# Kernel optimization log

Hardware: AMD Instinct MI355X
Metric: run time of the kernel (lower is better)

## Reference

```python
import jax, jax.numpy as jnp
import numpy as np
from jax import lax


def _bayer_kernels():
    # 5 fixed 3x3 interpolation stencils (identity, plus-avg, cross-avg, h-avg, v-avg)
    k5 = np.array([
        [[0, 0, 0], [0, 1, 0], [0, 0, 0]],
        [[0, .25, 0], [.25, 0, .25], [0, .25, 0]],
        [[.25, 0, .25], [0, 0, 0], [.25, 0, .25]],
        [[0, 0, 0], [.5, 0, .5], [0, 0, 0]],
        [[0, .5, 0], [0, 0, 0], [0, .5, 0]],
    ], dtype=np.float32)  # (5,3,3)
    # 4 fixed (3,5) selection matrices (1x1 convs per Bayer quadrant)
    sel = np.array([
        [[0, 0, 1, 0, 0], [0, 1, 0, 0, 0], [1, 0, 0, 0, 0]],
        [[0, 0, 0, 0, 1], [1, 0, 0, 0, 0], [0, 0, 0, 1, 0]],
        [[0, 0, 0, 1, 0], [1, 0, 0, 0, 0], [0, 0, 0, 0, 1]],
        [[1, 0, 0, 0, 0], [0, 1, 0, 0, 0], [0, 0, 1, 0, 0]],
    ], dtype=np.float32)  # (4,3,5)
    return jnp.asarray(k5), jnp.asarray(sel)


def setup_inputs() -> dict:
    key = jax.random.key(0)
    x = jax.random.uniform(key, (2, 1, 4096, 4096), dtype=jnp.float32) * 255.0
    k5, sel = _bayer_kernels()
    return {"x": x, "kernels5": k5, "sel": sel}


def reference(x, kernels5, sel):
    n, _, h, w = x.shape
    x_pad = jnp.pad(x, ((0, 0), (0, 0), (1, 1), (1, 1)), mode="reflect")
    # 3x3 stencil bank: (N,1,H+2,W+2) -> (N,5,H,W)
    xc = lax.conv_general_dilated(
        x_pad, kernels5.reshape(5, 1, 3, 3), window_strides=(1, 1),
        padding="VALID", dimension_numbers=("NCHW", "OIHW", "NCHW"))
    h2, w2 = h // 2, w // 2
    # pixel-unshuffle (DCR order): (N,5,H,W) -> (N, 2,2, 5, H/2, W/2) -> (N,4,5,H/2,W/2)
    u = xc.reshape(n, 5, h2, 2, w2, 2).transpose(0, 3, 5, 1, 2, 4).reshape(n, 4, 5, h2, w2)
    # per-quadrant 1x1 selection conv: (N,4,3,H/2,W/2)
    e = jnp.einsum("qos,nqsxy->nqoxy", sel, u)
    # pixel-shuffle (DCR order): (N,4,3,H/2,W/2) -> (N,3,H,W)
    y = e.reshape(n, 2, 2, 3, h2, w2).transpose(0, 3, 4, 1, 5, 2).reshape(n, 3, h, w)
    return y
```

## Files before the change

kernel.cpp:

```cpp
#include <hip/hip_runtime.h>


#define IMG_H 4096
#define IMG_W 4096

typedef float v4f __attribute__((ext_vector_type(4)));

__device__ __forceinline__ void load_win(const float* __restrict__ rowp, int j,
                                         int lane, float w[6]) {
    const float4 v = *(const float4*)(rowp + j);
    w[1] = v.x; w[2] = v.y; w[3] = v.z; w[4] = v.w;
    float left  = __shfl_up(v.w, 1);
    float right = __shfl_down(v.x, 1);
    if (lane == 0)  left  = (j == 0) ? v.y : rowp[j - 1];
    if (lane == 63) right = (j == IMG_W - 4) ? v.z : rowp[j + 4];
    w[0] = left; w[5] = right;
}

__global__ __launch_bounds__(256) void bayer_demosaic_kernel(
    const float* __restrict__ x, float* __restrict__ out) {
    const int jg   = blockIdx.x * blockDim.x + threadIdx.x;
    const int r    = blockIdx.y << 1;
    const int n    = blockIdx.z;
    const int j    = jg << 2;
    const int lane = threadIdx.x & 63;

    const float* xn = x + (size_t)n * IMG_H * IMG_W;

    const int rm = (r == 0) ? 1 : r - 1;
    const int rp = (r == IMG_H - 2) ? IMG_H - 2 : r + 2;

    const float* rowA = xn + (size_t)rm * IMG_W;
    const float* rowB = xn + (size_t)r  * IMG_W;
    const float* rowC = xn + (size_t)(r + 1) * IMG_W;
    const float* rowD = xn + (size_t)rp * IMG_W;

    float a[6], b[6], c[6], d[6];
    load_win(rowA, j, lane, a);
    load_win(rowB, j, lane, b);
    load_win(rowC, j, lane, c);
    load_win(rowD, j, lane, d);

    float e0[4], e1[4], e2[4];
    float f0[4], f1[4], f2[4];
#pragma unroll
    for (int k = 0; k < 4; ++k) {
        {
            const float center = b[k + 1];
            const float plus   = 0.25f * (a[k + 1] + c[k + 1] + b[k] + b[k + 2]);
            const float cross  = 0.25f * (a[k] + a[k + 2] + c[k] + c[k + 2]);
            const float havg   = 0.5f  * (b[k] + b[k + 2]);
            const float vavg   = 0.5f  * (a[k + 1] + c[k + 1]);
            if ((k & 1) == 0) { e0[k] = cross; e1[k] = plus;   e2[k] = center; }
            else              { e0[k] = vavg;  e1[k] = center; e2[k] = havg;   }
        }
        {
            const float center = c[k + 1];
            const float plus   = 0.25f * (b[k + 1] + d[k + 1] + c[k] + c[k + 2]);
            const float cross  = 0.25f * (b[k] + b[k + 2] + d[k] + d[k + 2]);
            const float havg   = 0.5f  * (c[k] + c[k + 2]);
            const float vavg   = 0.5f  * (b[k + 1] + d[k + 1]);
            if ((k & 1) == 0) { f0[k] = havg;   f1[k] = center; f2[k] = vavg;  }
            else              { f0[k] = center; f1[k] = plus;   f2[k] = cross; }
        }
    }

    float* on = out + (size_t)n * 3 * IMG_H * IMG_W;
    const size_t plane = (size_t)IMG_H * IMG_W;
    const size_t off0  = (size_t)r * IMG_W + j;
    const size_t off1  = off0 + IMG_W;

    v4f t;
    t = (v4f){e0[0], e0[1], e0[2], e0[3]};
    __builtin_nontemporal_store(t, (v4f*)(on + off0));
    t = (v4f){f0[0], f0[1], f0[2], f0[3]};
    __builtin_nontemporal_store(t, (v4f*)(on + off1));
    t = (v4f){e1[0], e1[1], e1[2], e1[3]};
    __builtin_nontemporal_store(t, (v4f*)(on + plane + off0));
    t = (v4f){f1[0], f1[1], f1[2], f1[3]};
    __builtin_nontemporal_store(t, (v4f*)(on + plane + off1));
    t = (v4f){e2[0], e2[1], e2[2], e2[3]};
    __builtin_nontemporal_store(t, (v4f*)(on + 2 * plane + off0));
    t = (v4f){f2[0], f2[1], f2[2], f2[3]};
    __builtin_nontemporal_store(t, (v4f*)(on + 2 * plane + off1));
}

extern "C" void kernel_launch(void* const* d_in, const int* in_sizes, int n_in,
                              void* d_out, int out_size, void* d_ws, size_t ws_size,
                              hipStream_t stream) {
    const float* x = (const float*)d_in[0];
    float* out = (float*)d_out;

    const int N = 2;
    dim3 block(256, 1, 1);
    dim3 grid(IMG_W / 4 / 256, IMG_H / 2, N);
    bayer_demosaic_kernel<<<grid, block, 0, stream>>>(x, out);
}
```

Measured before the change: 488.6 us.

## Process multiple row pairs per thread with sliding window reuse

Each thread now loops over several consecutive row pairs and carries the previous two rows' windows forward, so each input row is loaded about once instead of twice. The grid's y-dimension shrinks accordingly. Output stores switch from nontemporal builtins to plain float4 stores. This reduces redundant global/L2 reads and per-block overhead, but lowers parallelism and may change write caching behaviour.

```diff
diff --git a/kernel.cpp b/kernel.cpp
--- a/kernel.cpp
+++ b/kernel.cpp
@@ -3,8 +3,7 @@
 
 #define IMG_H 4096
 #define IMG_W 4096
-
-typedef float v4f __attribute__((ext_vector_type(4)));
+#define T_PAIRS 8
 
 __device__ __forceinline__ void load_win(const float* __restrict__ rowp, int j,
                                          int lane, float w[6]) {
@@ -20,69 +19,64 @@
 __global__ __launch_bounds__(256) void bayer_demosaic_kernel(
     const float* __restrict__ x, float* __restrict__ out) {
     const int jg   = blockIdx.x * blockDim.x + threadIdx.x;
-    const int r    = blockIdx.y << 1;
-    const int n    = blockIdx.z;
     const int j    = jg << 2;
     const int lane = threadIdx.x & 63;
+    const int n    = blockIdx.z;
+    int r = blockIdx.y * (2 * T_PAIRS);
 
     const float* xn = x + (size_t)n * IMG_H * IMG_W;
+    float* on       = out + (size_t)n * 3 * IMG_H * IMG_W;
+    const size_t plane = (size_t)IMG_H * IMG_W;
 
-    const int rm = (r == 0) ? 1 : r - 1;
-    const int rp = (r == IMG_H - 2) ? IMG_H - 2 : r + 2;
-
-    const float* rowA = xn + (size_t)rm * IMG_W;
-    const float* rowB = xn + (size_t)r  * IMG_W;
-    const float* rowC = xn + (size_t)(r + 1) * IMG_W;
-    const float* rowD = xn + (size_t)rp * IMG_W;
-
-    float a[6], b[6], c[6], d[6];
-    load_win(rowA, j, lane, a);
-    load_win(rowB, j, lane, b);
-    load_win(rowC, j, lane, c);
-    load_win(rowD, j, lane, d);
-
-    float e0[4], e1[4], e2[4];
-    float f0[4], f1[4], f2[4];
-#pragma unroll
-    for (int k = 0; k < 4; ++k) {
-        {
-            const float center = b[k + 1];
-            const float plus   = 0.25f * (a[k + 1] + c[k + 1] + b[k] + b[k + 2]);
-            const float cross  = 0.25f * (a[k] + a[k + 2] + c[k] + c[k + 2]);
-            const float havg   = 0.5f  * (b[k] + b[k + 2]);
-            const float vavg   = 0.5f  * (a[k + 1] + c[k + 1]);
-            if ((k & 1) == 0) { e0[k] = cross; e1[k] = plus;   e2[k] = center; }
-            else              { e0[k] = vavg;  e1[k] = center; e2[k] = havg;   }
-        }
-        {
-            const float center = c[k + 1];
-            const float plus   = 0.25f * (b[k + 1] + d[k + 1] + c[k] + c[k + 2]);
-            const float cross  = 0.25f * (b[k] + b[k + 2] + d[k] + d[k + 2]);
-            const float havg   = 0.5f  * (c[k] + c[k + 2]);
-            const float vavg   = 0.5f  * (b[k + 1] + d[k + 1]);
-            if ((k & 1) == 0) { f0[k] = havg;   f1[k] = center; f2[k] = vavg;  }
-            else              { f0[k] = center; f1[k] = plus;   f2[k] = cross; }
-        }
+    float A[6], B[6], C[6], D[6];
+    {
+        const int rm = (r == 0) ? 1 : r - 1;
+        load_win(xn + (size_t)rm * IMG_W, j, lane, A);
+        load_win(xn + (size_t)r  * IMG_W, j, lane, B);
     }
 
-    float* on = out + (size_t)n * 3 * IMG_H * IMG_W;
-    const size_t plane = (size_t)IMG_H * IMG_W;
-    const size_t off0  = (size_t)r * IMG_W + j;
-    const size_t off1  = off0 + IMG_W;
+#pragma unroll
+    for (int t = 0; t < T_PAIRS; ++t, r += 2) {
+        const int rp = (r == IMG_H - 2) ? IMG_H - 2 : r + 2;
+        load_win(xn + (size_t)(r + 1) * IMG_W, j, lane, C);
+        load_win(xn + (size_t)rp * IMG_W, j, lane, D);
 
-    v4f t;
-    t = (v4f){e0[0], e0[1], e0[2], e0[3]};
-    __builtin_nontemporal_store(t, (v4f*)(on + off0));
-    t = (v4f){f0[0], f0[1], f0[2], f0[3]};
-    __builtin_nontemporal_store(t, (v4f*)(on + off1));
-    t = (v4f){e1[0], e1[1], e1[2], e1[3]};
-    __builtin_nontemporal_store(t, (v4f*)(on + plane + off0));
-    t = (v4f){f1[0], f1[1], f1[2], f1[3]};
-    __builtin_nontemporal_store(t, (v4f*)(on + plane + off1));
-    t = (v4f){e2[0], e2[1], e2[2], e2[3]};
-    __builtin_nontemporal_store(t, (v4f*)(on + 2 * plane + off0));
-    t = (v4f){f2[0], f2[1], f2[2], f2[3]};
-    __builtin_nontemporal_store(t, (v4f*)(on + 2 * plane + off1));
+        float e0[4], e1[4], e2[4];
+        float f0[4], f1[4], f2[4];
+#pragma unroll
+        for (int k = 0; k < 4; ++k) {
+            {
+                const float center = B[k + 1];
+                const float plus   = 0.25f * (A[k + 1] + C[k + 1] + B[k] + B[k + 2]);
+                const float cross  = 0.25f * (A[k] + A[k + 2] + C[k] + C[k + 2]);
+                const float havg   = 0.5f  * (B[k] + B[k + 2]);
+                const float vavg   = 0.5f  * (A[k + 1] + C[k + 1]);
+                if ((k & 1) == 0) { e0[k] = cross; e1[k] = plus;   e2[k] = center; }
+                else              { e0[k] = vavg;  e1[k] = center; e2[k] = havg;   }
+            }
+            {
+                const float center = C[k + 1];
+                const float plus   = 0.25f * (B[k + 1] + D[k + 1] + C[k] + C[k + 2]);
+                const float cross  = 0.25f * (B[k] + B[k + 2] + D[k] + D[k + 2]);
+                const float havg   = 0.5f  * (C[k] + C[k + 2]);
+                const float vavg   = 0.5f  * (B[k + 1] + D[k + 1]);
+                if ((k & 1) == 0) { f0[k] = havg;   f1[k] = center; f2[k] = vavg;  }
+                else              { f0[k] = center; f1[k] = plus;   f2[k] = cross; }
+            }
+        }
+
+        const size_t off0 = (size_t)r * IMG_W + j;
+        const size_t off1 = off0 + IMG_W;
+        *(float4*)(on + off0)             = make_float4(e0[0], e0[1], e0[2], e0[3]);
+        *(float4*)(on + off1)             = make_float4(f0[0], f0[1], f0[2], f0[3]);
+        *(float4*)(on + plane + off0)     = make_float4(e1[0], e1[1], e1[2], e1[3]);
+        *(float4*)(on + plane + off1)     = make_float4(f1[0], f1[1], f1[2], f1[3]);
+        *(float4*)(on + 2 * plane + off0) = make_float4(e2[0], e2[1], e2[2], e2[3]);
+        *(float4*)(on + 2 * plane + off1) = make_float4(f2[0], f2[1], f2[2], f2[3]);
+
+#pragma unroll
+        for (int q = 0; q < 6; ++q) { A[q] = C[q]; B[q] = D[q]; }
+    }
 }
 
 extern "C" void kernel_launch(void* const* d_in, const int* in_sizes, int n_in,
@@ -93,6 +87,6 @@
 
     const int N = 2;
     dim3 block(256, 1, 1);
-    dim3 grid(IMG_W / 4 / 256, IMG_H / 2, N);
+    dim3 grid(IMG_W / 4 / 256, IMG_H / (2 * T_PAIRS), N);
     bayer_demosaic_kernel<<<grid, block, 0, stream>>>(x, out);
 }
```

After: 500.9 us. +2.5%, slower.
